# Kernel optimization log

Hardware: AMD Instinct MI355X
Metric: run time of the kernel (lower is better)

The kernel has to match this reference:

```python
import jax, jax.numpy as jnp
import numpy as np

NUM_HEADS = 16
NUM_KV_HEADS = 4
HEAD_DIM = 128
ROPE_THETA = 10000.0
LN_EPS = 1e-5


def rotate_half(x):
    h = x.shape[-1] // 2
    return jnp.concatenate([-x[..., h:], x[..., :h]], axis=-1)


def setup_inputs() -> dict:
    key = jax.random.key(0)
    ks = jax.random.split(key, 12)
    B, S, H = 2, 2048, 2048
    qdim = NUM_HEADS * HEAD_DIM          # 2048
    kvdim = NUM_KV_HEADS * HEAD_DIM      # 512
    s = 1.0 / np.sqrt(H)
    return {
        'hidden_states': jax.random.normal(ks[0], (B, S, H), jnp.float32),
        'position_ids': jnp.arange(S, dtype=jnp.int32).reshape(1, S),
        'Wq': jax.random.normal(ks[1], (H, qdim), jnp.float32) * s,
        'Wk': jax.random.normal(ks[2], (H, kvdim), jnp.float32) * s,
        'Wv': jax.random.normal(ks[3], (H, kvdim), jnp.float32) * s,
        'Wo': jax.random.normal(ks[4], (qdim, H), jnp.float32) * (1.0 / np.sqrt(qdim)),
        'Wg1': jax.random.normal(ks[5], (H, NUM_HEADS), jnp.float32) * s,
        'bg1': jnp.zeros((NUM_HEADS,), jnp.float32),
        'Wg2': jax.random.normal(ks[6], (H, NUM_HEADS), jnp.float32) * s,
        'bg2': jnp.zeros((NUM_HEADS,), jnp.float32),
        'ln_gamma': jnp.ones((HEAD_DIM,), jnp.float32),
        'ln_beta': jnp.zeros((HEAD_DIM,), jnp.float32),
    }


def reference(hidden_states, position_ids, Wq, Wk, Wv, Wo, Wg1, bg1, Wg2, bg2, ln_gamma, ln_beta):
    B, S, H = hidden_states.shape
    dt = hidden_states.dtype

    # q/k/v projections -> (B, heads, S, head_dim)
    q = (hidden_states @ Wq).reshape(B, S, NUM_HEADS, HEAD_DIM).transpose(0, 2, 1, 3)
    k = (hidden_states @ Wk).reshape(B, S, NUM_KV_HEADS, HEAD_DIM).transpose(0, 2, 1, 3)
    v = (hidden_states @ Wv).reshape(B, S, NUM_KV_HEADS, HEAD_DIM).transpose(0, 2, 1, 3)

    # Llama RoPE
    inv_freq = 1.0 / (ROPE_THETA ** (jnp.arange(0, HEAD_DIM, 2, dtype=jnp.float32) / HEAD_DIM))
    freqs = position_ids.astype(jnp.float32)[..., None] * inv_freq  # (1, S, hd/2)
    emb = jnp.concatenate([freqs, freqs], axis=-1)                  # (1, S, hd)
    cos = jnp.cos(emb)[:, None].astype(dt)                          # (1, 1, S, hd)
    sin = jnp.sin(emb)[:, None].astype(dt)
    q = q * cos + rotate_half(q) * sin
    k = k * cos + rotate_half(k) * sin

    # GQA: repeat kv heads
    n_rep = NUM_HEADS // NUM_KV_HEADS
    k = jnp.repeat(k, n_rep, axis=1)
    v = jnp.repeat(v, n_rep, axis=1)

    # per-token per-head gates: (B, S, heads) -> (B, heads, S, 1)
    g1 = jax.nn.sigmoid(hidden_states @ Wg1 + bg1).transpose(0, 2, 1)[..., None]
    g2 = jax.nn.sigmoid(hidden_states @ Wg2 + bg2).transpose(0, 2, 1)[..., None]

    # value gating (weight_proj2)
    v = v * g2

    # causal softmax attention
    scores = jnp.einsum('bhqd,bhkd->bhqk', q, k) / np.sqrt(HEAD_DIM)
    causal = jnp.tril(jnp.ones((S, S), bool))
    scores = jnp.where(causal[None, None], scores, jnp.finfo(jnp.float32).min)
    probs = jax.nn.softmax(scores.astype(jnp.float32), axis=-1).astype(dt)
    o = jnp.einsum('bhqk,bhkd->bhqd', probs, v)  # (B, heads, S, hd)

    # per-head LayerNorm over head_dim, then output gating (weight_proj)
    mu = jnp.mean(o, axis=-1, keepdims=True)
    var = jnp.mean(jnp.square(o - mu), axis=-1, keepdims=True)
    o = (o - mu) / jnp.sqrt(var + LN_EPS) * ln_gamma + ln_beta
    o = o * g1

    o = o.transpose(0, 2, 1, 3).reshape(B, S, NUM_HEADS * HEAD_DIM)
    return o @ Wo
```

## Files before the change

kernel.cpp:

```cpp
#include <hip/hip_runtime.h>
#include <hip/hip_bf16.h>
#include <stdint.h>
#include <string.h>

using bf16 = __hip_bfloat16;
typedef __attribute__((ext_vector_type(8))) short bf16x8;
typedef __attribute__((ext_vector_type(4))) float f32x4;

#define DEV static __device__ __forceinline__

DEV bf16 tobf(float f) { return __float2bfloat16(f); }
DEV float tof(bf16 h) { return __bfloat162float(h); }

DEV void gload_lds16(const void* g, void* l) {
  __builtin_amdgcn_global_load_lds((__attribute__((address_space(1))) void*)g,
                                   (__attribute__((address_space(3))) void*)l,
                                   16, 0, 0);
}


__global__ void transpose_cast_k(const float* __restrict__ src, bf16* __restrict__ dst,
                                 int K, int N) {
  __shared__ float tile[32][33];
  int kb = blockIdx.x * 32, nb = blockIdx.y * 32;
  int tx = threadIdx.x, ty = threadIdx.y;
#pragma unroll
  for (int i = 0; i < 32; i += 8)
    tile[ty + i][tx] = src[(size_t)(kb + ty + i) * N + nb + tx];
  __syncthreads();
#pragma unroll
  for (int i = 0; i < 32; i += 8)
    dst[(size_t)(nb + ty + i) * K + kb + tx] = tobf(tile[tx][ty + i]);
}

__global__ void gw_transpose_k(const float* __restrict__ Wg1, const float* __restrict__ Wg2,
                               bf16* __restrict__ dstbase) {
  int g = blockIdx.x >> 4, r = blockIdx.x & 15;
  const float* src = g ? Wg2 : Wg1;
  bf16* dst = dstbase + (size_t)(3072 + g * 16 + r) * 2048;
  for (int k = threadIdx.x; k < 2048; k += 256) dst[k] = tobf(src[(size_t)k * 16 + r]);
}

__global__ void cast_x_k(const float* __restrict__ src, bf16* __restrict__ dst) {
  int i = blockIdx.x * blockDim.x + threadIdx.x;
  float4 v = ((const float4*)src)[i];
  bf16 t[4] = {tobf(v.x), tobf(v.y), tobf(v.z), tobf(v.w)};
  uint2 p; __builtin_memcpy(&p, t, 8);
  ((uint2*)dst)[i] = p;
}

__global__ void rope_table_k(const int* __restrict__ pos, float* __restrict__ cosT,
                             float* __restrict__ sinT) {
  int s = blockIdx.x, i = threadIdx.x;
  double inv = exp(-((double)(2 * i) / 128.0) * log(10000.0));
  float f = (float)pos[s] * (float)inv;
  cosT[s * 64 + i] = cosf(f);
  sinT[s * 64 + i] = sinf(f);
}

__global__ __launch_bounds__(256) void rope_apply_k(
    bf16* __restrict__ qkv, const float* __restrict__ cosT, const float* __restrict__ sinT) {
  int idx = blockIdx.x * 256 + threadIdx.x;
  int c = idx & 7, hh = idx >> 3;
  int head = hh % 20, t = hh / 20;
  int s = t & 2047;
  size_t base = (size_t)t * 3072 + (head < 16 ? head * 128 : 2048 + (head - 16) * 128);
  int d0 = c * 8;
  bf16x8 lo = *(const bf16x8*)(qkv + base + d0);
  bf16x8 hi = *(const bf16x8*)(qkv + base + d0 + 64);
  float4 c0 = *(const float4*)(cosT + s * 64 + d0);
  float4 c1 = *(const float4*)(cosT + s * 64 + d0 + 4);
  float4 s0 = *(const float4*)(sinT + s * 64 + d0);
  float4 s1 = *(const float4*)(sinT + s * 64 + d0 + 4);
  float cs[8] = {c0.x, c0.y, c0.z, c0.w, c1.x, c1.y, c1.z, c1.w};
  float sn[8] = {s0.x, s0.y, s0.z, s0.w, s1.x, s1.y, s1.z, s1.w};
  bf16x8 olo, ohi;
#pragma unroll
  for (int j = 0; j < 8; j++) {
    float a = tof(((const bf16*)&lo)[j]), b = tof(((const bf16*)&hi)[j]);
    ((bf16*)&olo)[j] = tobf(a * cs[j] - b * sn[j]);
    ((bf16*)&ohi)[j] = tobf(b * cs[j] + a * sn[j]);
  }
  *(bf16x8*)(qkv + base + d0) = olo;
  *(bf16x8*)(qkv + base + d0 + 64) = ohi;
}

__global__ __launch_bounds__(256, 2) void gemm_qkv_k(
    const bf16* __restrict__ A, const bf16* __restrict__ Bt, bf16* __restrict__ qkv,
    float* __restrict__ g1t, float* __restrict__ g2t,
    const float* __restrict__ bg1, const float* __restrict__ bg2) {
  constexpr int BK = 32, K = 2048;
  __shared__ bf16 sA[2][128 * BK];
  __shared__ bf16 sB[2][128 * BK];
  const int tid = threadIdx.x, wave = tid >> 6, lane = tid & 63;
  const int lhi = lane >> 4, llo = lane & 15;
  const int wm = wave >> 1, wn = wave & 1;
  const int bm = blockIdx.y, bn = blockIdx.x;
  const bf16* Ag = A + (size_t)bm * 128 * K;
  const bf16* Bg = Bt + (size_t)bn * 128 * K;

  f32x4 acc[4][4];
#pragma unroll
  for (int m = 0; m < 4; m++)
#pragma unroll
    for (int n = 0; n < 4; n++) acc[m][n] = f32x4{0.f, 0.f, 0.f, 0.f};

  auto stage = [&](int buf, int kt) {
#pragma unroll
    for (int i = 0; i < 2; i++) {
      int c = i * 256 + tid, row = c >> 2, c8 = c & 3;
      gload_lds16(Ag + (size_t)row * K + kt * BK + c8 * 8, &sA[buf][c * 8]);
    }
#pragma unroll
    for (int i = 0; i < 2; i++) {
      int c = i * 256 + tid, row = c >> 2, c8 = c & 3;
      gload_lds16(Bg + (size_t)row * K + kt * BK + c8 * 8, &sB[buf][c * 8]);
    }
  };

  const int NT = K / BK;
  stage(0, 0);
  for (int kt = 0; kt < NT; kt++) {
    __syncthreads();
    if (kt + 1 < NT) stage((kt + 1) & 1, kt + 1);
    const bf16* a_ = sA[kt & 1];
    const bf16* b_ = sB[kt & 1];
    bf16x8 af[4], bfr[4];
#pragma unroll
    for (int m = 0; m < 4; m++)
      af[m] = *(const bf16x8*)&a_[(wm * 64 + m * 16 + llo) * BK + lhi * 8];
#pragma unroll
    for (int n = 0; n < 4; n++)
      bfr[n] = *(const bf16x8*)&b_[(wn * 64 + n * 16 + llo) * BK + lhi * 8];
#pragma unroll
    for (int m = 0; m < 4; m++)
#pragma unroll
      for (int n = 0; n < 4; n++)
        acc[m][n] = __builtin_amdgcn_mfma_f32_16x16x32_bf16(af[m], bfr[n], acc[m][n], 0, 0, 0);
  }

  const int r0 = bm * 128 + wm * 64, c0 = bn * 128 + wn * 64;
#pragma unroll
  for (int m = 0; m < 4; m++)
#pragma unroll
    for (int n = 0; n < 4; n++) {
      int col = c0 + n * 16 + llo;
#pragma unroll
      for (int r = 0; r < 4; r++) {
        int row = r0 + m * 16 + lhi * 4 + r;
        if (col < 3072) {
          qkv[(size_t)row * 3072 + col] = tobf(acc[m][n][r]);
        } else if (col < 3104) {
          int idx = col - 3072, hh = idx & 15;
          float b = (idx < 16) ? bg1[hh] : bg2[hh];
          float v = 1.f / (1.f + __expf(-(acc[m][n][r] + b)));
          ((idx < 16) ? g1t : g2t)[(size_t)hh * 4096 + row] = v;
        }
      }
    }
}

__global__ __launch_bounds__(256, 2) void gemm_out_k(
    const bf16* __restrict__ A, const bf16* __restrict__ Bt, float* __restrict__ C,
    int M, int N, int K) {
  constexpr int BK = 32;
  __shared__ bf16 sA[2][128 * BK];
  __shared__ bf16 sB[2][128 * BK];
  const int tid = threadIdx.x, wave = tid >> 6, lane = tid & 63;
  const int lhi = lane >> 4, llo = lane & 15;
  const int wm = wave >> 1, wn = wave & 1;
  const int bm = blockIdx.y, bn = blockIdx.x;
  const bf16* Ag = A + (size_t)bm * 128 * K;
  const bf16* Bg = Bt + (size_t)bn * 128 * K;

  f32x4 acc[4][4];
#pragma unroll
  for (int m = 0; m < 4; m++)
#pragma unroll
    for (int n = 0; n < 4; n++) acc[m][n] = f32x4{0.f, 0.f, 0.f, 0.f};

  auto stage = [&](int buf, int kt) {
#pragma unroll
    for (int i = 0; i < 2; i++) {
      int c = i * 256 + tid, row = c >> 2, c8 = c & 3;
      gload_lds16(Ag + (size_t)row * K + kt * BK + c8 * 8, &sA[buf][c * 8]);
    }
#pragma unroll
    for (int i = 0; i < 2; i++) {
      int c = i * 256 + tid, row = c >> 2, c8 = c & 3;
      gload_lds16(Bg + (size_t)row * K + kt * BK + c8 * 8, &sB[buf][c * 8]);
    }
  };

  const int NT = K / BK;
  stage(0, 0);
  for (int kt = 0; kt < NT; kt++) {
    __syncthreads();
    if (kt + 1 < NT) stage((kt + 1) & 1, kt + 1);
    const bf16* a_ = sA[kt & 1];
    const bf16* b_ = sB[kt & 1];
    bf16x8 af[4], bfr[4];
#pragma unroll
    for (int m = 0; m < 4; m++)
      af[m] = *(const bf16x8*)&a_[(wm * 64 + m * 16 + llo) * BK + lhi * 8];
#pragma unroll
    for (int n = 0; n < 4; n++)
      bfr[n] = *(const bf16x8*)&b_[(wn * 64 + n * 16 + llo) * BK + lhi * 8];
#pragma unroll
    for (int m = 0; m < 4; m++)
#pragma unroll
      for (int n = 0; n < 4; n++)
        acc[m][n] = __builtin_amdgcn_mfma_f32_16x16x32_bf16(af[m], bfr[n], acc[m][n], 0, 0, 0);
  }

  const int r0 = bm * 128 + wm * 64, c0 = bn * 128 + wn * 64;
#pragma unroll
  for (int m = 0; m < 4; m++)
#pragma unroll
    for (int n = 0; n < 4; n++)
#pragma unroll
      for (int r = 0; r < 4; r++)
        C[(size_t)(r0 + m * 16 + lhi * 4 + r) * N + (c0 + n * 16 + llo)] = acc[m][n][r];
}

DEV void finalize_store(const f32x4 (&o)[8], int wave, int lhi, int llo, int tid,
                        int h, int qt, size_t tok0,
                        const float* __restrict__ g1t, const float* __restrict__ lng,
                        const float* __restrict__ lnb, bf16* sK, bf16* __restrict__ aout) {
  float sum[4] = {0, 0, 0, 0}, sq[4] = {0, 0, 0, 0};
#pragma unroll
  for (int dt = 0; dt < 8; dt++)
#pragma unroll
    for (int r = 0; r < 4; r++) {
      float v = o[dt][r];
      sum[r] += v;
      sq[r] += v * v;
    }
  float mu[4], rstd[4];
#pragma unroll
  for (int r = 0; r < 4; r++) {
    float s1 = sum[r], s2 = sq[r];
    s1 += __shfl_xor(s1, 1); s1 += __shfl_xor(s1, 2); s1 += __shfl_xor(s1, 4); s1 += __shfl_xor(s1, 8);
    s2 += __shfl_xor(s2, 1); s2 += __shfl_xor(s2, 2); s2 += __shfl_xor(s2, 4); s2 += __shfl_xor(s2, 8);
    float m_ = s1 * (1.f / 128.f);
    float var = s2 * (1.f / 128.f) - m_ * m_;
    mu[r] = m_;
    rstd[r] = rsqrtf(var + 1e-5f);
  }
  __syncthreads();
#pragma unroll
  for (int r = 0; r < 4; r++) {
    int lrow = wave * 16 + lhi * 4 + r;
    float gg = g1t[(size_t)h * 4096 + tok0 + qt * 64 + lrow];
#pragma unroll
    for (int dt = 0; dt < 8; dt++) {
      int d = dt * 16 + llo;
      float v = (o[dt][r] - mu[r]) * rstd[r] * lng[d] + lnb[d];
      sK[lrow * 128 + d] = tobf(v * gg);
    }
  }
  __syncthreads();
#pragma unroll
  for (int i = 0; i < 4; i++) {
    int c = i * 256 + tid, lr = c >> 4, c8 = c & 15;
    *(uint4*)(aout + (tok0 + qt * 64 + lr) * 2048 + h * 128 + c8 * 8) =
        *(const uint4*)&sK[lr * 128 + c8 * 8];
  }
}

DEV int pid_base(int qt) {
  return qt < 8 ? qt : qt < 16 ? 2 * qt - 8 : qt < 24 ? 3 * qt - 24 : 4 * qt - 48;
}

__device__ const unsigned char UNIT_TAB[80] = {
  124,125,126,127,
  120,121,122, 116,117,118, 112,113,114,
  108,109,110, 104,105,106, 100,101,102,
   96, 97, 98,  92, 93, 94,
   88, 89,  84, 85,  80, 81,  76, 77,
   72, 73,  68, 69,  64, 65,  60, 61,
   56, 52, 48, 44, 40, 36, 32, 28,
  123, 90, 57, 24,
  119, 86, 53, 20,
  115, 82, 49, 16,
  111, 78, 45, 12,
  107, 74, 41,  8,
  103, 70, 37,  4,
   99, 66, 33,  0
};

__global__ __launch_bounds__(256, 2) void attn_split_k(
    const bf16* __restrict__ qkv, const float* __restrict__ g2t,
    const float* __restrict__ g1t, const float* __restrict__ lng,
    const float* __restrict__ lnb,
    float* __restrict__ pO, float* __restrict__ pML, bf16* __restrict__ aout) {
  constexpr int S = 2048, LD = 3072;
  const int bid = blockIdx.x;
  const int g = bid & 7, j = bid >> 3;
  const int hp = j & 1, u = j >> 1;
  const int e = UNIT_TAB[u];
  const int qt = e >> 2, s = e & 3;
  const int k0 = s * 8, k1 = min(s * 8 + 8, qt + 1);
  const bool partial = (qt >= 8);

  const int b = g >> 2, kvh = g & 3, h0 = kvh * 4 + hp * 2;
  const int tid = threadIdx.x, wave = tid >> 6, lane = tid & 63;
  const int lhi = lane >> 4, llo = lane & 15;
  const size_t tok0 = (size_t)b * S;

  __shared__ bf16 sK[64 * 128];
  __shared__ bf16 sV[128 * 64];
  __shared__ bf16 sP[4][2][16][72];

  const int qrow0 = qt * 64 + wave * 16;

  bf16x8 qf[2][4];
#pragma unroll
  for (int hh = 0; hh < 2; hh++) {
    const bf16* qg = qkv + (tok0 + qrow0 + llo) * LD + (h0 + hh) * 128;
#pragma unroll
    for (int dc = 0; dc < 4; dc++) qf[hh][dc] = *(const bf16x8*)(qg + dc * 32 + lhi * 8);
  }

  f32x4 oacc[2][8];
#pragma unroll
  for (int hh = 0; hh < 2; hh++)
#pragma unroll
    for (int i = 0; i < 8; i++) oacc[hh][i] = f32x4{0.f, 0.f, 0.f, 0.f};
  float mrow[2][4], lrow[2][4];
#pragma unroll
  for (int hh = 0; hh < 2; hh++)
#pragma unroll
    for (int r = 0; r < 4; r++) { mrow[hh][r] = -1e30f; lrow[hh][r] = 0.f; }
  const float scale = 0.08838834764831845f;

  uint4 kreg[4];
  bf16x8 vreg[4];
  float gvreg[2];
  const int vdg = tid >> 4;
  const int vkg = tid & 15;

  auto issue_loads = [&](int kt) {
#pragma unroll
    for (int i = 0; i < 4; i++) {
      int c = i * 256 + tid, row = c >> 4, c8 = c & 15;
      kreg[i] = *(const uint4*)(qkv + (tok0 + kt * 64 + row) * LD + 2048 + kvh * 128 + c8 * 8);
    }
#pragma unroll
    for (int r = 0; r < 4; r++)
      vreg[r] = *(const bf16x8*)(qkv + (tok0 + kt * 64 + vkg * 4 + r) * LD + 2560 +
                                 kvh * 128 + vdg * 8);
#pragma unroll
    for (int hh = 0; hh < 2; hh++)
      gvreg[hh] = g2t[(size_t)(h0 + hh) * 4096 + tok0 + kt * 64 + lane];
  };

  auto write_lds = [&]() {
#pragma unroll
    for (int i = 0; i < 4; i++) {
      int c = i * 256 + tid, row = c >> 4, c8 = c & 15;
      int eidx = (row * 128 + c8 * 8) ^ ((row & 7) << 3);
      *(uint4*)&sK[eidx] = kreg[i];
    }
#pragma unroll
    for (int e2 = 0; e2 < 8; e2++) {
      int d = vdg * 8 + e2;
      uint32_t lo = (uint32_t)(unsigned short)vreg[0][e2] |
                    ((uint32_t)(unsigned short)vreg[1][e2] << 16);
      uint32_t hi = (uint32_t)(unsigned short)vreg[2][e2] |
                    ((uint32_t)(unsigned short)vreg[3][e2] << 16);
      int eidx = (d * 64 + vkg * 4) ^ (e2 << 3);
      uint2 pk; pk.x = lo; pk.y = hi;
      *(uint2*)&sV[eidx] = pk;
    }
  };

  issue_loads(k0);
  for (int kt = k0; kt < k1; kt++) {
    __syncthreads();
    write_lds();
    float gv0 = gvreg[0], gv1 = gvreg[1];
    if (kt + 1 < k1) issue_loads(kt + 1);
    __syncthreads();

    const bool diag = (kt == qt);
#pragma unroll
    for (int hh = 0; hh < 2; hh++) {
      f32x4 sc[4];
#pragma unroll
      for (int ct = 0; ct < 4; ct++) {
        f32x4 acc = f32x4{0.f, 0.f, 0.f, 0.f};
#pragma unroll
        for (int dc = 0; dc < 4; dc++) {
          int row = ct * 16 + llo;
          bf16x8 kf = *(const bf16x8*)&sK[(row * 128 + dc * 32 + lhi * 8) ^ ((row & 7) << 3)];
          acc = __builtin_amdgcn_mfma_f32_16x16x32_bf16(qf[hh][dc], kf, acc, 0, 0, 0);
        }
        sc[ct] = acc;
      }
      float pm[4] = {-1e30f, -1e30f, -1e30f, -1e30f};
#pragma unroll
      for (int ct = 0; ct < 4; ct++) {
        int kv = kt * 64 + ct * 16 + llo;
#pragma unroll
        for (int r = 0; r < 4; r++) {
          float s_ = sc[ct][r] * scale;
          if (diag && kv > qrow0 + lhi * 4 + r) s_ = -1e30f;
          sc[ct][r] = s_;
          pm[r] = fmaxf(pm[r], s_);
        }
      }
#pragma unroll
      for (int r = 0; r < 4; r++) {
        float v = pm[r];
        v = fmaxf(v, __shfl_xor(v, 1));
        v = fmaxf(v, __shfl_xor(v, 2));
        v = fmaxf(v, __shfl_xor(v, 4));
        v = fmaxf(v, __shfl_xor(v, 8));
        pm[r] = v;
      }
      int need = 0;
#pragma unroll
      for (int r = 0; r < 4; r++) need |= (pm[r] > mrow[hh][r]) ? 1 : 0;
      if (__any(need)) {
#pragma unroll
        for (int r = 0; r < 4; r++) {
          float mnew = fmaxf(mrow[hh][r], pm[r]);
          float al = __expf(mrow[hh][r] - mnew);
          mrow[hh][r] = mnew;
          lrow[hh][r] *= al;
#pragma unroll
          for (int i = 0; i < 8; i++) oacc[hh][i][r] *= al;
        }
      }
      float gv = hh ? gv1 : gv0;
      float g2v[4];
#pragma unroll
      for (int ct = 0; ct < 4; ct++) g2v[ct] = __shfl(gv, ct * 16 + llo);
      float rs[4] = {0.f, 0.f, 0.f, 0.f};
#pragma unroll
      for (int ct = 0; ct < 4; ct++) {
#pragma unroll
        for (int r = 0; r < 4; r++) {
          float p = __expf(sc[ct][r] - mrow[hh][r]);
          rs[r] += p;
          sP[wave][hh][lhi * 4 + r][ct * 16 + llo] = tobf(p * g2v[ct]);
        }
      }
#pragma unroll
      for (int r = 0; r < 4; r++) {
        float v = rs[r];
        v += __shfl_xor(v, 1); v += __shfl_xor(v, 2); v += __shfl_xor(v, 4); v += __shfl_xor(v, 8);
        lrow[hh][r] += v;
      }
    }
#pragma unroll
    for (int kc = 0; kc < 2; kc++) {
      bf16x8 pf0 = *(const bf16x8*)&sP[wave][0][llo][kc * 32 + lhi * 8];
      bf16x8 pf1 = *(const bf16x8*)&sP[wave][1][llo][kc * 32 + lhi * 8];
#pragma unroll
      for (int dt = 0; dt < 8; dt++) {
        int d = dt * 16 + llo;
        bf16x8 vf = *(const bf16x8*)&sV[(d * 64 + kc * 32 + lhi * 8) ^ ((d & 7) << 3)];
        oacc[0][dt] = __builtin_amdgcn_mfma_f32_16x16x32_bf16(pf0, vf, oacc[0][dt], 0, 0, 0);
        oacc[1][dt] = __builtin_amdgcn_mfma_f32_16x16x32_bf16(pf1, vf, oacc[1][dt], 0, 0, 0);
      }
    }
  }

  if (partial) {
    const int pid = pid_base(qt) + s;
#pragma unroll
    for (int hh = 0; hh < 2; hh++) {
      const int sub = (g * 2 + hp) * 2 + hh;
      f32x4* dst = (f32x4*)pO + (size_t)(pid * 32 + sub) * 2048;
#pragma unroll
      for (int dt = 0; dt < 8; dt++)
        dst[(wave * 8 + dt) * 64 + lane] = oacc[hh][dt];
      if (llo == 0) {
#pragma unroll
        for (int r = 0; r < 4; r++) {
          int row = wave * 16 + lhi * 4 + r;
          float* pm = pML + ((size_t)(pid * 32 + sub) * 64 + row) * 2;
          pm[0] = mrow[hh][r];
          pm[1] = lrow[hh][r];
        }
      }
    }
  } else {
#pragma unroll
    for (int hh = 0; hh < 2; hh++) {
      float inv[4];
#pragma unroll
      for (int r = 0; r < 4; r++) inv[r] = 1.f / lrow[hh][r];
      f32x4 o[8];
#pragma unroll
      for (int dt = 0; dt < 8; dt++)
#pragma unroll
        for (int r = 0; r < 4; r++) o[dt][r] = oacc[hh][dt][r] * inv[r];
      finalize_store(o, wave, lhi, llo, tid, h0 + hh, qt, tok0, g1t, lng, lnb, sK, aout);
    }
  }
}

__global__ __launch_bounds__(256) void attn_combine_k(
    const float* __restrict__ pO, const float* __restrict__ pML,
    const float* __restrict__ g1t, const float* __restrict__ lng,
    const float* __restrict__ lnb, bf16* __restrict__ aout) {
  __shared__ bf16 sK[64 * 128];
  const int bid = blockIdx.x;
  const int g = bid & 7, j = bid >> 3;
  const int hp = j & 1, qtc = j >> 1;
  const int qt = 8 + qtc;
  const int ns = (qt < 16) ? 2 : (qt < 24) ? 3 : 4;
  const int p0id = pid_base(qt);
  const int b = g >> 2, kvh = g & 3, h0 = kvh * 4 + hp * 2;
  const int tid = threadIdx.x, wave = tid >> 6, lane = tid & 63;
  const int lhi = lane >> 4, llo = lane & 15;
  const size_t tok0 = (size_t)b * 2048;
#pragma unroll
  for (int hh = 0; hh < 2; hh++) {
    const int sub = (g * 2 + hp) * 2 + hh;
    float w[4][4], inv[4];
#pragma unroll
    for (int r = 0; r < 4; r++) {
      int row = wave * 16 + lhi * 4 + r;
      float m[4], l[4], ms = -1e30f;
#pragma unroll
      for (int sp = 0; sp < 4; sp++)
        if (sp < ns) {
          const float* q = pML + ((size_t)((p0id + sp) * 32 + sub) * 64 + row) * 2;
          m[sp] = q[0]; l[sp] = q[1];
          ms = fmaxf(ms, m[sp]);
        }
      float L = 0.f;
#pragma unroll
      for (int sp = 0; sp < 4; sp++)
        if (sp < ns) { w[sp][r] = __expf(m[sp] - ms); L += w[sp][r] * l[sp]; }
      inv[r] = 1.f / L;
    }
    f32x4 o[8];
#pragma unroll
    for (int dt = 0; dt < 8; dt++) {
      f32x4 a = f32x4{0.f, 0.f, 0.f, 0.f};
#pragma unroll
      for (int sp = 0; sp < 4; sp++)
        if (sp < ns) {
          f32x4 c = ((const f32x4*)pO + (size_t)((p0id + sp) * 32 + sub) * 2048)
                        [(wave * 8 + dt) * 64 + lane];
#pragma unroll
          for (int r = 0; r < 4; r++) a[r] += w[sp][r] * c[r];
        }
#pragma unroll
      for (int r = 0; r < 4; r++) o[dt][r] = a[r] * inv[r];
    }
    finalize_store(o, wave, lhi, llo, tid, h0 + hh, qt, tok0, g1t, lng, lnb, sK, aout);
  }
}

extern "C" void kernel_launch(void* const* d_in, const int* in_sizes, int n_in,
                              void* d_out, int out_size, void* d_ws, size_t ws_size,
                              hipStream_t stream) {
  (void)in_sizes; (void)n_in; (void)out_size; (void)ws_size;
  const float* X   = (const float*)d_in[0];
  const int*   pos = (const int*)d_in[1];
  const float* Wq  = (const float*)d_in[2];
  const float* Wk  = (const float*)d_in[3];
  const float* Wv  = (const float*)d_in[4];
  const float* Wo  = (const float*)d_in[5];
  const float* Wg1 = (const float*)d_in[6];
  const float* bg1 = (const float*)d_in[7];
  const float* Wg2 = (const float*)d_in[8];
  const float* bg2 = (const float*)d_in[9];
  const float* lng = (const float*)d_in[10];
  const float* lnb = (const float*)d_in[11];

  char* ws = (char*)d_ws;
  size_t off = 0;
  auto alloc = [&](size_t bytes) {
    void* p = ws + off;
    off += (bytes + 255) & ~(size_t)255;
    return p;
  };
  bf16*  WT   = (bf16*)alloc(3200ull * 2048 * 2);
  bf16*  WoT  = (bf16*)alloc(2048ull * 2048 * 2);
  bf16*  Xbf  = (bf16*)alloc(4096ull * 2048 * 2);
  bf16*  qkv  = (bf16*)alloc(4096ull * 3072 * 2);
  bf16*  attn = (bf16*)alloc(4096ull * 2048 * 2);
  float* cosT = (float*)alloc(2048ull * 64 * 4);
  float* sinT = (float*)alloc(2048ull * 64 * 4);
  float* g1t  = (float*)alloc(16ull * 4096 * 4);
  float* g2t  = (float*)alloc(16ull * 4096 * 4);
  float* pO   = (float*)alloc(80ull * 32 * 8192 * 4);
  float* pML  = (float*)alloc(80ull * 32 * 64 * 2 * 4);

  dim3 tb(32, 8);
  transpose_cast_k<<<dim3(64, 64), tb, 0, stream>>>(Wq, WT, 2048, 2048);
  transpose_cast_k<<<dim3(64, 16), tb, 0, stream>>>(Wk, WT + 2048ull * 2048, 2048, 512);
  transpose_cast_k<<<dim3(64, 16), tb, 0, stream>>>(Wv, WT + 2560ull * 2048, 2048, 512);
  transpose_cast_k<<<dim3(64, 64), tb, 0, stream>>>(Wo, WoT, 2048, 2048);
  gw_transpose_k<<<32, 256, 0, stream>>>(Wg1, Wg2, WT);
  cast_x_k<<<8192, 256, 0, stream>>>(X, Xbf);
  rope_table_k<<<2048, 64, 0, stream>>>(pos, cosT, sinT);

  gemm_qkv_k<<<dim3(25, 32), 256, 0, stream>>>(Xbf, WT, qkv, g1t, g2t, bg1, bg2);
  rope_apply_k<<<2560, 256, 0, stream>>>(qkv, cosT, sinT);
  attn_split_k<<<1280, 256, 0, stream>>>(qkv, g2t, g1t, lng, lnb, pO, pML, attn);
  attn_combine_k<<<384, 256, 0, stream>>>(pO, pML, g1t, lng, lnb, attn);
  gemm_out_k<<<dim3(16, 32), 256, 0, stream>>>(attn, WoT, (float*)d_out, 4096, 2048, 2048);
}
```

Baseline: 312.1 us.

## Merge weight transposes, swizzle GEMM block order, and shrink attention P buffer

Folds the four weight transpose-cast launches into one kernel, which removes launch overhead. Both GEMMs now use a 1D grid with a block-index swizzle that groups blocks across the 8 XCDs, aiming for better L2 reuse of A/B tiles. In attention, the per-wave P staging buffer is cut to one head and uses an XOR-swizzled layout instead of padding. The PV MFMAs now run inside the per-head loop, which lowers LDS use but adds more dependency between the softmax and MFMA phases.

New measurement: 317.0 us. Within noise of the previous version (+1.6%).

```diff
diff --git a/kernel.cpp b/kernel.cpp
--- a/kernel.cpp
+++ b/kernel.cpp
@@ -19,10 +19,18 @@
 }
 
 
-__global__ void transpose_cast_k(const float* __restrict__ src, bf16* __restrict__ dst,
-                                 int K, int N) {
+__global__ void transpose_all_k(const float* __restrict__ Wq, const float* __restrict__ Wk,
+                                const float* __restrict__ Wv, const float* __restrict__ Wo,
+                                bf16* __restrict__ WT, bf16* __restrict__ WoT) {
   __shared__ float tile[32][33];
-  int kb = blockIdx.x * 32, nb = blockIdx.y * 32;
+  int t = blockIdx.x;
+  const float* src; bf16* dst; int N, tt;
+  if (t < 4096)      { src = Wq; dst = WT;                 N = 2048; tt = t; }
+  else if (t < 5120) { src = Wk; dst = WT + 2048ull * 2048; N = 512; tt = t - 4096; }
+  else if (t < 6144) { src = Wv; dst = WT + 2560ull * 2048; N = 512; tt = t - 5120; }
+  else               { src = Wo; dst = WoT;                N = 2048; tt = t - 6144; }
+  int sh = (N == 2048) ? 6 : 4;
+  int kb = (tt >> sh) << 5, nb = (tt & ((1 << sh) - 1)) << 5;
   int tx = threadIdx.x, ty = threadIdx.y;
 #pragma unroll
   for (int i = 0; i < 32; i += 8)
@@ -30,7 +38,7 @@
   __syncthreads();
 #pragma unroll
   for (int i = 0; i < 32; i += 8)
-    dst[(size_t)(nb + ty + i) * K + kb + tx] = tobf(tile[tx][ty + i]);
+    dst[(size_t)(nb + ty + i) * 2048 + kb + tx] = tobf(tile[tx][ty + i]);
 }
 
 __global__ void gw_transpose_k(const float* __restrict__ Wg1, const float* __restrict__ Wg2,
@@ -95,7 +103,9 @@
   const int tid = threadIdx.x, wave = tid >> 6, lane = tid & 63;
   const int lhi = lane >> 4, llo = lane & 15;
   const int wm = wave >> 1, wn = wave & 1;
-  const int bm = blockIdx.y, bn = blockIdx.x;
+  const int bid = blockIdx.x;
+  const int swz = (bid & 7) * 100 + (bid >> 3);
+  const int bm = swz & 31, bn = swz >> 5;
   const bf16* Ag = A + (size_t)bm * 128 * K;
   const bf16* Bg = Bt + (size_t)bn * 128 * K;
 
@@ -162,14 +172,16 @@
 
 __global__ __launch_bounds__(256, 2) void gemm_out_k(
     const bf16* __restrict__ A, const bf16* __restrict__ Bt, float* __restrict__ C,
-    int M, int N, int K) {
+    int N, int K) {
   constexpr int BK = 32;
   __shared__ bf16 sA[2][128 * BK];
   __shared__ bf16 sB[2][128 * BK];
   const int tid = threadIdx.x, wave = tid >> 6, lane = tid & 63;
   const int lhi = lane >> 4, llo = lane & 15;
   const int wm = wave >> 1, wn = wave & 1;
-  const int bm = blockIdx.y, bn = blockIdx.x;
+  const int bid = blockIdx.x;
+  const int swz = (bid & 7) * 64 + (bid >> 3);
+  const int bm = swz & 31, bn = swz >> 5;
   const bf16* Ag = A + (size_t)bm * 128 * K;
   const bf16* Bg = Bt + (size_t)bn * 128 * K;
 
@@ -310,7 +322,7 @@
 
   __shared__ bf16 sK[64 * 128];
   __shared__ bf16 sV[128 * 64];
-  __shared__ bf16 sP[4][2][16][72];
+  __shared__ bf16 sP[4][16 * 64];
 
   const int qrow0 = qt * 64 + wave * 16;
 
@@ -444,7 +456,8 @@
         for (int r = 0; r < 4; r++) {
           float p = __expf(sc[ct][r] - mrow[hh][r]);
           rs[r] += p;
-          sP[wave][hh][lhi * 4 + r][ct * 16 + llo] = tobf(p * g2v[ct]);
+          int row = lhi * 4 + r;
+          sP[wave][(row * 64 + ct * 16 + llo) ^ ((row & 7) << 3)] = tobf(p * g2v[ct]);
         }
       }
 #pragma unroll
@@ -453,17 +466,15 @@
         v += __shfl_xor(v, 1); v += __shfl_xor(v, 2); v += __shfl_xor(v, 4); v += __shfl_xor(v, 8);
         lrow[hh][r] += v;
       }
-    }
-#pragma unroll
-    for (int kc = 0; kc < 2; kc++) {
-      bf16x8 pf0 = *(const bf16x8*)&sP[wave][0][llo][kc * 32 + lhi * 8];
-      bf16x8 pf1 = *(const bf16x8*)&sP[wave][1][llo][kc * 32 + lhi * 8];
-#pragma unroll
-      for (int dt = 0; dt < 8; dt++) {
-        int d = dt * 16 + llo;
-        bf16x8 vf = *(const bf16x8*)&sV[(d * 64 + kc * 32 + lhi * 8) ^ ((d & 7) << 3)];
-        oacc[0][dt] = __builtin_amdgcn_mfma_f32_16x16x32_bf16(pf0, vf, oacc[0][dt], 0, 0, 0);
-        oacc[1][dt] = __builtin_amdgcn_mfma_f32_16x16x32_bf16(pf1, vf, oacc[1][dt], 0, 0, 0);
+#pragma unroll
+      for (int kc = 0; kc < 2; kc++) {
+        bf16x8 pf = *(const bf16x8*)&sP[wave][(llo * 64 + kc * 32 + lhi * 8) ^ ((llo & 7) << 3)];
+#pragma unroll
+        for (int dt = 0; dt < 8; dt++) {
+          int d = dt * 16 + llo;
+          bf16x8 vf = *(const bf16x8*)&sV[(d * 64 + kc * 32 + lhi * 8) ^ ((d & 7) << 3)];
+          oacc[hh][dt] = __builtin_amdgcn_mfma_f32_16x16x32_bf16(pf, vf, oacc[hh][dt], 0, 0, 0);
+        }
       }
     }
   }
@@ -594,18 +605,14 @@
   float* pO   = (float*)alloc(80ull * 32 * 8192 * 4);
   float* pML  = (float*)alloc(80ull * 32 * 64 * 2 * 4);
 
-  dim3 tb(32, 8);
-  transpose_cast_k<<<dim3(64, 64), tb, 0, stream>>>(Wq, WT, 2048, 2048);
-  transpose_cast_k<<<dim3(64, 16), tb, 0, stream>>>(Wk, WT + 2048ull * 2048, 2048, 512);
-  transpose_cast_k<<<dim3(64, 16), tb, 0, stream>>>(Wv, WT + 2560ull * 2048, 2048, 512);
-  transpose_cast_k<<<dim3(64, 64), tb, 0, stream>>>(Wo, WoT, 2048, 2048);
+  transpose_all_k<<<10240, dim3(32, 8), 0, stream>>>(Wq, Wk, Wv, Wo, WT, WoT);
   gw_transpose_k<<<32, 256, 0, stream>>>(Wg1, Wg2, WT);
   cast_x_k<<<8192, 256, 0, stream>>>(X, Xbf);
   rope_table_k<<<2048, 64, 0, stream>>>(pos, cosT, sinT);
 
-  gemm_qkv_k<<<dim3(25, 32), 256, 0, stream>>>(Xbf, WT, qkv, g1t, g2t, bg1, bg2);
+  gemm_qkv_k<<<800, 256, 0, stream>>>(Xbf, WT, qkv, g1t, g2t, bg1, bg2);
   rope_apply_k<<<2560, 256, 0, stream>>>(qkv, cosT, sinT);
   attn_split_k<<<1280, 256, 0, stream>>>(qkv, g2t, g1t, lng, lnb, pO, pML, attn);
   attn_combine_k<<<384, 256, 0, stream>>>(pO, pML, g1t, lng, lnb, attn);
-  gemm_out_k<<<dim3(16, 32), 256, 0, stream>>>(attn, WoT, (float*)d_out, 4096, 2048, 2048);
-}
+  gemm_out_k<<<512, 256, 0, stream>>>(attn, WoT, (float*)d_out, 2048, 2048);
+}
```
